# Optimization experiments

Measured on AMD Instinct MI355X. Metric: run time of the kernel, lower is better.

The kernel has to match this reference:

```python
import jax, jax.numpy as jnp
import numpy as np

NH = 16   # n_heads
HD = 64   # head_size
EMB = 1024  # n_embd = NH * HD
B, T = 4, 2048


def setup_inputs() -> dict:
    key = jax.random.key(0)
    k1, k2, k3 = jax.random.split(key, 3)
    x = jax.random.normal(k1, (B, T, EMB), dtype=jnp.float32)
    # torch Linear(in, out, bias=False): weight [out,in]; we store transposed [in,out]
    W_attn = jax.random.normal(k2, (EMB, 3 * NH * HD), dtype=jnp.float32) * (EMB ** -0.5)
    W_proj = jax.random.normal(k3, (NH * HD, EMB), dtype=jnp.float32) * ((NH * HD) ** -0.5)
    b_proj = jnp.zeros((EMB,), dtype=jnp.float32)
    return {"x": x, "W_attn": W_attn, "W_proj": W_proj, "b_proj": b_proj}


def reference(x, W_attn, W_proj, b_proj):
    Bq, Tq, C = x.shape
    qkv = x @ W_attn                      # [B,T,3*Nh*H]
    qs, ks, vs = jnp.split(qkv, 3, axis=2)
    def to_heads(t):                      # [B,T,Nh*H] -> [B,Nh,T,H]
        return t.reshape(Bq, Tq, NH, HD).transpose(0, 2, 1, 3)
    q, k, v = to_heads(qs), to_heads(ks), to_heads(vs)
    scores = jnp.einsum('bnth,bnsh->bnts', q, k) * (HD ** -0.5)  # [B,Nh,T,T]
    causal = jnp.tril(jnp.ones((Tq, Tq), dtype=bool))
    scores = jnp.where(causal, scores, -jnp.inf)
    attn = jax.nn.softmax(scores, axis=-1)
    # dropout is identity in eval mode
    y = jnp.einsum('bnts,bnsh->bnth', attn, v)                   # [B,Nh,T,H]
    y = y.transpose(0, 2, 1, 3).reshape(Bq, Tq, NH * HD)
    return y @ W_proj + b_proj
```

## Files before the change

kernel.cpp:

```cpp
#include <hip/hip_runtime.h>
#include <hip/hip_bf16.h>

#define NH 16
#define HD 64
#define EMB 1024
#define BB 4
#define TT 2048
#define MTOT (BB*TT)
#define N1 (3*NH*HD)
#define KD EMB

#define BM 128
#define BN 128
#define BK 32

typedef __bf16 bf16x8 __attribute__((ext_vector_type(8)));
typedef __bf16 bf16x4 __attribute__((ext_vector_type(4)));
typedef float  f32x4  __attribute__((ext_vector_type(4)));
typedef __hip_bfloat16 hbf;

__device__ __forceinline__ void async_copy16(const hbf* g, hbf* l) {
    __builtin_amdgcn_global_load_lds(
        (const __attribute__((address_space(1))) void*)g,
        (__attribute__((address_space(3))) void*)l, 16, 0, 0);
}

__device__ __forceinline__ bf16x4 pack4(float x0, float x1, float x2, float x3) {
    union { bf16x4 v; hbf a[4]; } u;
    u.a[0] = __float2bfloat16(x0);
    u.a[1] = __float2bfloat16(x1);
    u.a[2] = __float2bfloat16(x2);
    u.a[3] = __float2bfloat16(x3);
    return u.v;
}


__global__ void f32_to_bf16(const float* __restrict__ in, hbf* __restrict__ out, int n) {
    int i = blockIdx.x * blockDim.x + threadIdx.x;
    if (i < n) out[i] = __float2bfloat16(in[i]);
}

__global__ void f32_to_bf16_T(const float* __restrict__ in, hbf* __restrict__ out, int R, int C) {
    int i = blockIdx.x * blockDim.x + threadIdx.x;
    if (i < R * C) {
        int r = i / C, c = i % C;
        out[(size_t)c * R + r] = __float2bfloat16(in[i]);
    }
}


#define GEMM_STAGE(Sdst, Gsrc, ld)                                            \
    {                                                                         \
        _Pragma("unroll")                                                     \
        for (int q = 0; q < 2; ++q) {                                         \
            int e = q * 2048 + tid * 8;                                       \
            int row = e >> 5, col = e & 31;                                   \
            async_copy16(Gsrc + (size_t)row * (ld) + col,                     \
                         Sdst + q * 2048 + (tid & ~63) * 8);                  \
        }                                                                     \
    }

__global__ __launch_bounds__(256) void gemm_qkv(
    const hbf* __restrict__ A, const hbf* __restrict__ Bt,
    hbf* __restrict__ qh, hbf* __restrict__ kh, hbf* __restrict__ vt)
{
    __shared__ __align__(16) hbf As[BM * BK];
    __shared__ __align__(16) hbf Bs[BN * BK];
    int tid = threadIdx.x;
    int wv = tid >> 6, lane = tid & 63;
    int g = lane >> 4, c = lane & 15;
    int wr = wv >> 1, wc = wv & 1;
    int bn = blockIdx.x % (N1 / BN);
    int bm = blockIdx.x / (N1 / BN);
    int m0 = bm * BM, n0 = bn * BN;

    f32x4 acc[4][4];
    #pragma unroll
    for (int i = 0; i < 4; ++i)
        #pragma unroll
        for (int j = 0; j < 4; ++j) acc[i][j] = (f32x4){0.f, 0.f, 0.f, 0.f};

    for (int k0 = 0; k0 < KD; k0 += BK) {
        const hbf* Ag = A  + (size_t)m0 * KD + k0;
        const hbf* Bg = Bt + (size_t)n0 * KD + k0;
        GEMM_STAGE(As, Ag, KD);
        GEMM_STAGE(Bs, Bg, KD);
        __syncthreads();
        bf16x8 af[4], bf[4];
        #pragma unroll
        for (int mi = 0; mi < 4; ++mi)
            af[mi] = *(const bf16x8*)(As + (wr * 64 + mi * 16 + c) * BK + g * 8);
        #pragma unroll
        for (int ni = 0; ni < 4; ++ni)
            bf[ni] = *(const bf16x8*)(Bs + (wc * 64 + ni * 16 + c) * BK + g * 8);
        #pragma unroll
        for (int mi = 0; mi < 4; ++mi)
            #pragma unroll
            for (int ni = 0; ni < 4; ++ni)
                acc[mi][ni] = __builtin_amdgcn_mfma_f32_16x16x32_bf16(af[mi], bf[ni], acc[mi][ni], 0, 0, 0);
        __syncthreads();
    }

    int colbase = n0 + wc * 64;
    int which = colbase / (NH * HD);
    int h = (colbase % (NH * HD)) / HD;
    int b = m0 / TT;
    float scale = (which == 0) ? 0.125f : 1.0f;
    if (which < 2) {
        hbf* dst = (which == 0) ? qh : kh;
        dst += ((size_t)b * NH + h) * TT * HD;
        #pragma unroll
        for (int mi = 0; mi < 4; ++mi)
            #pragma unroll
            for (int ni = 0; ni < 4; ++ni) {
                int d = ni * 16 + c;
                #pragma unroll
                for (int r = 0; r < 4; ++r) {
                    int t = (m0 + wr * 64 + mi * 16 + g * 4 + r) % TT;
                    dst[(size_t)t * HD + d] = __float2bfloat16(acc[mi][ni][r] * scale);
                }
            }
    } else {
        hbf* dst = vt + ((size_t)b * NH + h) * TT * HD;
        #pragma unroll
        for (int mi = 0; mi < 4; ++mi)
            #pragma unroll
            for (int ni = 0; ni < 4; ++ni) {
                int d = ni * 16 + c;
                #pragma unroll
                for (int r = 0; r < 4; ++r) {
                    int t = (m0 + wr * 64 + mi * 16 + g * 4 + r) % TT;
                    dst[(size_t)d * TT + t] = __float2bfloat16(acc[mi][ni][r]);
                }
            }
    }
}


__global__ __launch_bounds__(256, 2) void attn(
    const hbf* __restrict__ qh, const hbf* __restrict__ kh, const hbf* __restrict__ vt,
    hbf* __restrict__ y)
{
    __shared__ __align__(16) hbf Ks[64 * 64];
    __shared__ __align__(16) hbf Vs[64 * 64];
    __shared__ __align__(16) hbf Ps[4][2][16 * 64];

    int tid = threadIdx.x;
    int wv = tid >> 6, lane = tid & 63;
    int g = lane >> 4, c = lane & 15;
    int c7 = c & 7;

    int bh = blockIdx.x >> 3;
    int pi = blockIdx.x & 7;
    int b = bh >> 4, h = bh & 15;

    const hbf* Q = qh + (size_t)bh * TT * HD;
    const hbf* K = kh + (size_t)bh * TT * HD;
    const hbf* V = vt + (size_t)bh * TT * HD;

    #pragma unroll
    for (int pass = 0; pass < 2; ++pass) {
        int sst = pass ? (15 - pi) : pi;
        int qb = sst * 128;
        int qA = qb + wv * 32;
        int qB = qA + 16;
        int kendA = qA + 16, kendB = qA + 32;
        int kmax = qb + 128;

        bf16x8 aqA0 = *(const bf16x8*)(Q + (size_t)(qA + c) * HD + g * 8);
        bf16x8 aqA1 = *(const bf16x8*)(Q + (size_t)(qA + c) * HD + 32 + g * 8);
        bf16x8 aqB0 = *(const bf16x8*)(Q + (size_t)(qB + c) * HD + g * 8);
        bf16x8 aqB1 = *(const bf16x8*)(Q + (size_t)(qB + c) * HD + 32 + g * 8);

        float m_s[2] = {-1e30f, -1e30f}, l_s[2] = {0.f, 0.f};
        f32x4 o[2][4];
        #pragma unroll
        for (int qi = 0; qi < 2; ++qi)
            #pragma unroll
            for (int d = 0; d < 4; ++d) o[qi][d] = (f32x4){0.f, 0.f, 0.f, 0.f};

        for (int k0 = 0; k0 < kmax; k0 += 64) {
            __syncthreads();
            #pragma unroll
            for (int it = 0; it < 2; ++it) {
                int e = it * 2048 + tid * 8;
                int key = e >> 6, sblk = (e >> 3) & 7;
                int dblk = sblk ^ (key & 7);
                async_copy16(K + (size_t)(k0 + key) * HD + dblk * 8,
                             Ks + it * 2048 + (tid & ~63) * 8);
            }
            #pragma unroll
            for (int it = 0; it < 2; ++it) {
                int e = it * 2048 + tid * 8;
                int dim = e >> 6, sblk = (e >> 3) & 7;
                int kb = sblk ^ (dim & 7);
                async_copy16(V + (size_t)dim * TT + k0 + kb * 8,
                             Vs + it * 2048 + (tid & ~63) * 8);
            }
            __syncthreads();

            if (k0 < kendB) {
                f32x4 s[2][4];
                #pragma unroll
                for (int t = 0; t < 4; ++t) {
                    int kt = k0 + 16 * t;
                    if (kt < kendB) {
                        int rb = (16 * t + c) * 64;
                        bf16x8 kf0 = *(const bf16x8*)(Ks + rb + ((g ^ c7) << 3));
                        bf16x8 kf1 = *(const bf16x8*)(Ks + rb + (((4 + g) ^ c7) << 3));
                        if (kt < kendA) {
                            f32x4 a0 = (f32x4){0.f, 0.f, 0.f, 0.f};
                            a0 = __builtin_amdgcn_mfma_f32_16x16x32_bf16(kf0, aqA0, a0, 0, 0, 0);
                            a0 = __builtin_amdgcn_mfma_f32_16x16x32_bf16(kf1, aqA1, a0, 0, 0, 0);
                            if (kt == qA) {
                                #pragma unroll
                                for (int r = 0; r < 4; ++r)
                                    a0[r] = (g * 4 + r <= c) ? a0[r] : -1e30f;
                            }
                            s[0][t] = a0;
                        } else
                            s[0][t] = (f32x4){-1e30f, -1e30f, -1e30f, -1e30f};
                        f32x4 a1 = (f32x4){0.f, 0.f, 0.f, 0.f};
                        a1 = __builtin_amdgcn_mfma_f32_16x16x32_bf16(kf0, aqB0, a1, 0, 0, 0);
                        a1 = __builtin_amdgcn_mfma_f32_16x16x32_bf16(kf1, aqB1, a1, 0, 0, 0);
                        if (kt == qB) {
                            #pragma unroll
                            for (int r = 0; r < 4; ++r)
                                a1[r] = (g * 4 + r <= c) ? a1[r] : -1e30f;
                        }
                        s[1][t] = a1;
                    } else {
                        s[0][t] = (f32x4){-1e30f, -1e30f, -1e30f, -1e30f};
                        s[1][t] = (f32x4){-1e30f, -1e30f, -1e30f, -1e30f};
                    }
                }
                #pragma unroll
                for (int qi = 0; qi < 2; ++qi) {
                    int kend = qi ? kendB : kendA;
                    if (k0 < kend) {
                        f32x4 vmax = s[qi][0];
                        #pragma unroll
                        for (int t = 1; t < 4; ++t)
                            #pragma unroll
                            for (int r = 0; r < 4; ++r)
                                vmax[r] = fmaxf(vmax[r], s[qi][t][r]);
                        float mx = fmaxf(fmaxf(vmax[0], vmax[1]), fmaxf(vmax[2], vmax[3]));
                        mx = fmaxf(mx, __shfl_xor(mx, 16));
                        mx = fmaxf(mx, __shfl_xor(mx, 32));
                        float mn = fmaxf(m_s[qi], mx);
                        float al = __expf(m_s[qi] - mn);
                        m_s[qi] = mn;
                        f32x4 vsum = (f32x4){0.f, 0.f, 0.f, 0.f};
                        hbf* Pq = &Ps[wv][qi][0];
                        #pragma unroll
                        for (int t = 0; t < 4; ++t) {
                            f32x4 e;
                            #pragma unroll
                            for (int r = 0; r < 4; ++r) e[r] = __expf(s[qi][t][r] - mn);
                            vsum += e;
                            *(bf16x4*)(Pq + c * 64 + (((2 * t + (g >> 1)) ^ c7) << 3) + ((g & 1) << 2)) =
                                pack4(e[0], e[1], e[2], e[3]);
                        }
                        float sum = vsum[0] + vsum[1] + vsum[2] + vsum[3];
                        sum += __shfl_xor(sum, 16);
                        sum += __shfl_xor(sum, 32);
                        l_s[qi] = l_s[qi] * al + sum;
                        #pragma unroll
                        for (int d = 0; d < 4; ++d)
                            #pragma unroll
                            for (int r = 0; r < 4; ++r) o[qi][d][r] *= al;
                    }
                }
                #pragma unroll
                for (int sc = 0; sc < 2; ++sc) {
                    int kc = k0 + 32 * sc;
                    if (kc < kendB) {
                        bool lA = kc < kendA;
                        bf16x8 pfB = *(const bf16x8*)(&Ps[wv][1][0] + c * 64 + (((4 * sc + g) ^ c7) << 3));
                        bf16x8 pfA;
                        if (lA)
                            pfA = *(const bf16x8*)(&Ps[wv][0][0] + c * 64 + (((4 * sc + g) ^ c7) << 3));
                        #pragma unroll
                        for (int d = 0; d < 4; ++d) {
                            int dim = d * 16 + c;
                            bf16x8 vf = *(const bf16x8*)(Vs + dim * 64 + (((4 * sc + g) ^ c7) << 3));
                            if (lA)
                                o[0][d] = __builtin_amdgcn_mfma_f32_16x16x32_bf16(vf, pfA, o[0][d], 0, 0, 0);
                            o[1][d] = __builtin_amdgcn_mfma_f32_16x16x32_bf16(vf, pfB, o[1][d], 0, 0, 0);
                        }
                    }
                }
            }
        }

        #pragma unroll
        for (int qi = 0; qi < 2; ++qi) {
            int q0 = qA + qi * 16;
            float inv = 1.0f / l_s[qi];
            #pragma unroll
            for (int d = 0; d < 4; ++d) {
                *(bf16x4*)(y + (size_t)(b * TT + q0 + c) * EMB + h * HD + d * 16 + g * 4) =
                    pack4(o[qi][d][0] * inv, o[qi][d][1] * inv,
                          o[qi][d][2] * inv, o[qi][d][3] * inv);
            }
        }
    }
}


__global__ __launch_bounds__(256) void gemm_out(
    const hbf* __restrict__ A, const hbf* __restrict__ Bt,
    const float* __restrict__ bias, float* __restrict__ out)
{
    __shared__ __align__(16) hbf As[BM * BK];
    __shared__ __align__(16) hbf Bs[BN * BK];
    int tid = threadIdx.x;
    int wv = tid >> 6, lane = tid & 63;
    int g = lane >> 4, c = lane & 15;
    int wr = wv >> 1, wc = wv & 1;
    int bn = blockIdx.x % (EMB / BN);
    int bm = blockIdx.x / (EMB / BN);
    int m0 = bm * BM, n0 = bn * BN;

    f32x4 acc[4][4];
    #pragma unroll
    for (int i = 0; i < 4; ++i)
        #pragma unroll
        for (int j = 0; j < 4; ++j) acc[i][j] = (f32x4){0.f, 0.f, 0.f, 0.f};

    for (int k0 = 0; k0 < EMB; k0 += BK) {
        const hbf* Ag = A  + (size_t)m0 * EMB + k0;
        const hbf* Bg = Bt + (size_t)n0 * EMB + k0;
        GEMM_STAGE(As, Ag, EMB);
        GEMM_STAGE(Bs, Bg, EMB);
        __syncthreads();
        bf16x8 af[4], bf[4];
        #pragma unroll
        for (int mi = 0; mi < 4; ++mi)
            af[mi] = *(const bf16x8*)(As + (wr * 64 + mi * 16 + c) * BK + g * 8);
        #pragma unroll
        for (int ni = 0; ni < 4; ++ni)
            bf[ni] = *(const bf16x8*)(Bs + (wc * 64 + ni * 16 + c) * BK + g * 8);
        #pragma unroll
        for (int mi = 0; mi < 4; ++mi)
            #pragma unroll
            for (int ni = 0; ni < 4; ++ni)
                acc[mi][ni] = __builtin_amdgcn_mfma_f32_16x16x32_bf16(af[mi], bf[ni], acc[mi][ni], 0, 0, 0);
        __syncthreads();
    }

    #pragma unroll
    for (int mi = 0; mi < 4; ++mi)
        #pragma unroll
        for (int ni = 0; ni < 4; ++ni) {
            int col = n0 + wc * 64 + ni * 16 + c;
            float bv = bias[col];
            #pragma unroll
            for (int r = 0; r < 4; ++r) {
                int row = m0 + wr * 64 + mi * 16 + g * 4 + r;
                out[(size_t)row * EMB + col] = acc[mi][ni][r] + bv;
            }
        }
}


extern "C" void kernel_launch(void* const* d_in, const int* in_sizes, int n_in,
                              void* d_out, int out_size, void* d_ws, size_t ws_size,
                              hipStream_t stream)
{
    const float* x      = (const float*)d_in[0];
    const float* W_attn = (const float*)d_in[1];
    const float* W_proj = (const float*)d_in[2];
    const float* b_proj = (const float*)d_in[3];
    float* out = (float*)d_out;

    char* ws = (char*)d_ws;
    hbf* xb    = (hbf*)ws; ws += (size_t)MTOT * KD * 2;
    hbf* wab_t = (hbf*)ws; ws += (size_t)N1 * KD * 2;
    hbf* wpb_t = (hbf*)ws; ws += (size_t)EMB * EMB * 2;
    hbf* qh    = (hbf*)ws; ws += (size_t)MTOT * EMB * 2;
    hbf* kh    = (hbf*)ws; ws += (size_t)MTOT * EMB * 2;
    hbf* vt    = (hbf*)ws; ws += (size_t)MTOT * EMB * 2;
    hbf* yb    = (hbf*)ws; ws += (size_t)MTOT * EMB * 2;

    f32_to_bf16<<<(MTOT * KD + 255) / 256, 256, 0, stream>>>(x, xb, MTOT * KD);
    f32_to_bf16_T<<<(KD * N1 + 255) / 256, 256, 0, stream>>>(W_attn, wab_t, KD, N1);
    f32_to_bf16_T<<<(KD * EMB + 255) / 256, 256, 0, stream>>>(W_proj, wpb_t, KD, EMB);

    gemm_qkv<<<(MTOT / BM) * (N1 / BN), 256, 0, stream>>>(xb, wab_t, qh, kh, vt);
    attn<<<BB * NH * 8, 256, 0, stream>>>(qh, kh, vt, yb);
    gemm_out<<<(MTOT / BM) * (EMB / BN), 256, 0, stream>>>(yb, wpb_t, b_proj, out);
}
```

Measured before the change: 290.0 us.

## Retile attention to 64-query blocks with 128-key tiles and vectorize conversions

```diff
diff --git a/kernel.cpp b/kernel.cpp
--- a/kernel.cpp
+++ b/kernel.cpp
@@ -14,6 +14,8 @@
 #define BN 128
 #define BK 32
 
+#define QSCALE 0.18033688011112042f
+
 typedef __bf16 bf16x8 __attribute__((ext_vector_type(8)));
 typedef __bf16 bf16x4 __attribute__((ext_vector_type(4)));
 typedef float  f32x4  __attribute__((ext_vector_type(4)));
@@ -26,26 +28,35 @@
 }
 
 __device__ __forceinline__ bf16x4 pack4(float x0, float x1, float x2, float x3) {
-    union { bf16x4 v; hbf a[4]; } u;
-    u.a[0] = __float2bfloat16(x0);
-    u.a[1] = __float2bfloat16(x1);
-    u.a[2] = __float2bfloat16(x2);
-    u.a[3] = __float2bfloat16(x3);
+    union { bf16x4 v; __hip_bfloat162 h[2]; } u;
+    u.h[0] = __float22bfloat162_rn(float2{x0, x1});
+    u.h[1] = __float22bfloat162_rn(float2{x2, x3});
     return u.v;
 }
 
 
-__global__ void f32_to_bf16(const float* __restrict__ in, hbf* __restrict__ out, int n) {
+__global__ __launch_bounds__(256) void f32_to_bf16_v4(const float* __restrict__ in,
+                                                      hbf* __restrict__ out, int n4) {
     int i = blockIdx.x * blockDim.x + threadIdx.x;
-    if (i < n) out[i] = __float2bfloat16(in[i]);
-}
-
-__global__ void f32_to_bf16_T(const float* __restrict__ in, hbf* __restrict__ out, int R, int C) {
-    int i = blockIdx.x * blockDim.x + threadIdx.x;
-    if (i < R * C) {
-        int r = i / C, c = i % C;
-        out[(size_t)c * R + r] = __float2bfloat16(in[i]);
-    }
+    if (i < n4) {
+        float4 v = ((const float4*)in)[i];
+        *(bf16x4*)(out + 4 * (size_t)i) = pack4(v.x, v.y, v.z, v.w);
+    }
+}
+
+__global__ __launch_bounds__(256) void f32_to_bf16_T(const float* __restrict__ in,
+                                                     hbf* __restrict__ out, int R, int C) {
+    __shared__ float T[64][65];
+    int bc = blockIdx.x % (C / 64), br = blockIdx.x / (C / 64);
+    int r0 = br * 64, c0 = bc * 64;
+    int tr = threadIdx.x >> 6, tc = threadIdx.x & 63;
+    #pragma unroll
+    for (int i = 0; i < 16; ++i)
+        T[4 * i + tr][tc] = in[(size_t)(r0 + 4 * i + tr) * C + c0 + tc];
+    __syncthreads();
+    #pragma unroll
+    for (int i = 0; i < 16; ++i)
+        out[(size_t)(c0 + 4 * i + tr) * R + r0 + tc] = __float2bfloat16(T[tc][4 * i + tr]);
 }
 
 
@@ -105,7 +116,7 @@
     int which = colbase / (NH * HD);
     int h = (colbase % (NH * HD)) / HD;
     int b = m0 / TT;
-    float scale = (which == 0) ? 0.125f : 1.0f;
+    float scale = (which == 0) ? QSCALE : 1.0f;
     if (which < 2) {
         hbf* dst = (which == 0) ? qh : kh;
         dst += ((size_t)b * NH + h) * TT * HD;
@@ -137,35 +148,49 @@
 }
 
 
-__global__ __launch_bounds__(256, 2) void attn(
+__global__ __launch_bounds__(128, 2) void attn(
     const hbf* __restrict__ qh, const hbf* __restrict__ kh, const hbf* __restrict__ vt,
     hbf* __restrict__ y)
 {
-    __shared__ __align__(16) hbf Ks[64 * 64];
-    __shared__ __align__(16) hbf Vs[64 * 64];
-    __shared__ __align__(16) hbf Ps[4][2][16 * 64];
+    __shared__ __align__(16) hbf Ks[128 * 64];
+    __shared__ __align__(16) hbf Vs[2 * 64 * 64];
+    __shared__ __align__(16) hbf Ps[2][2][16 * 64];
 
     int tid = threadIdx.x;
     int wv = tid >> 6, lane = tid & 63;
     int g = lane >> 4, c = lane & 15;
     int c7 = c & 7;
 
-    int bh = blockIdx.x >> 3;
-    int pi = blockIdx.x & 7;
+    int bh = blockIdx.x >> 4;
+    int pi = blockIdx.x & 15;
     int b = bh >> 4, h = bh & 15;
 
     const hbf* Q = qh + (size_t)bh * TT * HD;
     const hbf* K = kh + (size_t)bh * TT * HD;
     const hbf* V = vt + (size_t)bh * TT * HD;
+    hbf* PqA = &Ps[wv][0][0];
+    hbf* PqB = &Ps[wv][1][0];
+
+    int koff[8], voff[8];
+    #pragma unroll
+    for (int it = 0; it < 8; ++it) {
+        int e = it * 1024 + tid * 8;
+        int key = e >> 6, sblk = (e >> 3) & 7;
+        koff[it] = key * HD + ((sblk ^ (key & 7)) << 3);
+        int ch = e >> 12, rem = e & 4095;
+        int dim = rem >> 6, kb8 = (rem >> 3) & 7;
+        voff[it] = dim * TT + ch * 64 + ((kb8 ^ (dim & 7)) << 3);
+    }
+    int ldsb = (tid & ~63) * 8;
 
     #pragma unroll
     for (int pass = 0; pass < 2; ++pass) {
-        int sst = pass ? (15 - pi) : pi;
-        int qb = sst * 128;
+        int sst = pass ? (31 - pi) : pi;
+        int qb = sst * 64;
         int qA = qb + wv * 32;
         int qB = qA + 16;
         int kendA = qA + 16, kendB = qA + 32;
-        int kmax = qb + 128;
+        int kmax = qb + 64;
 
         bf16x8 aqA0 = *(const bf16x8*)(Q + (size_t)(qA + c) * HD + g * 8);
         bf16x8 aqA1 = *(const bf16x8*)(Q + (size_t)(qA + c) * HD + 32 + g * 8);
@@ -179,114 +204,111 @@
             #pragma unroll
             for (int d = 0; d < 4; ++d) o[qi][d] = (f32x4){0.f, 0.f, 0.f, 0.f};
 
-        for (int k0 = 0; k0 < kmax; k0 += 64) {
+        for (int k0 = 0; k0 < kmax; k0 += 128) {
             __syncthreads();
             #pragma unroll
-            for (int it = 0; it < 2; ++it) {
-                int e = it * 2048 + tid * 8;
-                int key = e >> 6, sblk = (e >> 3) & 7;
-                int dblk = sblk ^ (key & 7);
-                async_copy16(K + (size_t)(k0 + key) * HD + dblk * 8,
-                             Ks + it * 2048 + (tid & ~63) * 8);
-            }
-            #pragma unroll
-            for (int it = 0; it < 2; ++it) {
-                int e = it * 2048 + tid * 8;
-                int dim = e >> 6, sblk = (e >> 3) & 7;
-                int kb = sblk ^ (dim & 7);
-                async_copy16(V + (size_t)dim * TT + k0 + kb * 8,
-                             Vs + it * 2048 + (tid & ~63) * 8);
-            }
+            for (int it = 0; it < 8; ++it)
+                async_copy16(K + (size_t)k0 * HD + koff[it], Ks + it * 1024 + ldsb);
+            #pragma unroll
+            for (int it = 0; it < 8; ++it)
+                async_copy16(V + k0 + voff[it], Vs + it * 1024 + ldsb);
             __syncthreads();
 
-            if (k0 < kendB) {
-                f32x4 s[2][4];
-                #pragma unroll
-                for (int t = 0; t < 4; ++t) {
-                    int kt = k0 + 16 * t;
-                    if (kt < kendB) {
-                        int rb = (16 * t + c) * 64;
-                        bf16x8 kf0 = *(const bf16x8*)(Ks + rb + ((g ^ c7) << 3));
-                        bf16x8 kf1 = *(const bf16x8*)(Ks + rb + (((4 + g) ^ c7) << 3));
-                        if (kt < kendA) {
-                            f32x4 a0 = (f32x4){0.f, 0.f, 0.f, 0.f};
-                            a0 = __builtin_amdgcn_mfma_f32_16x16x32_bf16(kf0, aqA0, a0, 0, 0, 0);
-                            a0 = __builtin_amdgcn_mfma_f32_16x16x32_bf16(kf1, aqA1, a0, 0, 0, 0);
-                            if (kt == qA) {
+            #pragma unroll
+            for (int ch = 0; ch < 2; ++ch) {
+                int c64 = k0 + ch * 64;
+                if (c64 < kendB) {
+                    f32x4 s[2][4];
+                    #pragma unroll
+                    for (int t = 0; t < 4; ++t) {
+                        int kt = c64 + 16 * t;
+                        if (kt < kendB) {
+                            int rb = (ch * 64 + 16 * t + c) * 64;
+                            bf16x8 kf0 = *(const bf16x8*)(Ks + rb + ((g ^ c7) << 3));
+                            bf16x8 kf1 = *(const bf16x8*)(Ks + rb + (((4 + g) ^ c7) << 3));
+                            if (kt < kendA) {
+                                f32x4 a = (f32x4){0.f, 0.f, 0.f, 0.f};
+                                a = __builtin_amdgcn_mfma_f32_16x16x32_bf16(kf0, aqA0, a, 0, 0, 0);
+                                a = __builtin_amdgcn_mfma_f32_16x16x32_bf16(kf1, aqA1, a, 0, 0, 0);
+                                if (kt == qA) {
+                                    #pragma unroll
+                                    for (int r = 0; r < 4; ++r)
+                                        a[r] = (g * 4 + r <= c) ? a[r] : -1e30f;
+                                }
+                                s[0][t] = a;
+                            } else
+                                s[0][t] = (f32x4){-1e30f, -1e30f, -1e30f, -1e30f};
+                            f32x4 a1 = (f32x4){0.f, 0.f, 0.f, 0.f};
+                            a1 = __builtin_amdgcn_mfma_f32_16x16x32_bf16(kf0, aqB0, a1, 0, 0, 0);
+                            a1 = __builtin_amdgcn_mfma_f32_16x16x32_bf16(kf1, aqB1, a1, 0, 0, 0);
+                            if (kt == qB) {
                                 #pragma unroll
                                 for (int r = 0; r < 4; ++r)
-                                    a0[r] = (g * 4 + r <= c) ? a0[r] : -1e30f;
+                                    a1[r] = (g * 4 + r <= c) ? a1[r] : -1e30f;
                             }
-                            s[0][t] = a0;
-                        } else
+                            s[1][t] = a1;
+                        } else {
                             s[0][t] = (f32x4){-1e30f, -1e30f, -1e30f, -1e30f};
-                        f32x4 a1 = (f32x4){0.f, 0.f, 0.f, 0.f};
-                        a1 = __builtin_amdgcn_mfma_f32_16x16x32_bf16(kf0, aqB0, a1, 0, 0, 0);
-                        a1 = __builtin_amdgcn_mfma_f32_16x16x32_bf16(kf1, aqB1, a1, 0, 0, 0);
-                        if (kt == qB) {
+                            s[1][t] = (f32x4){-1e30f, -1e30f, -1e30f, -1e30f};
+                        }
+                    }
+                    #pragma unroll
+                    for (int qi = 0; qi < 2; ++qi) {
+                        int kend = qi ? kendB : kendA;
+                        if (c64 < kend) {
+                            f32x4 vmax = s[qi][0];
                             #pragma unroll
-                            for (int r = 0; r < 4; ++r)
-                                a1[r] = (g * 4 + r <= c) ? a1[r] : -1e30f;
+                            for (int t = 1; t < 4; ++t)
+                                #pragma unroll
+                                for (int r = 0; r < 4; ++r)
+                                    vmax[r] = fmaxf(vmax[r], s[qi][t][r]);
+                            float mx = fmaxf(fmaxf(vmax[0], vmax[1]), fmaxf(vmax[2], vmax[3]));
+                            mx = fmaxf(mx, __shfl_xor(mx, 16));
+                            mx = fmaxf(mx, __shfl_xor(mx, 32));
+                            float mn = fmaxf(m_s[qi], mx);
+                            float al = exp2f(m_s[qi] - mn);
+                            m_s[qi] = mn;
+                            f32x4 vsum = (f32x4){0.f, 0.f, 0.f, 0.f};
+                            hbf* Pq = qi ? PqB : PqA;
+                            #pragma unroll
+                            for (int t = 0; t < 4; ++t) {
+                                f32x4 e;
+                                #pragma unroll
+                                for (int r = 0; r < 4; ++r) e[r] = exp2f(s[qi][t][r] - mn);
+                                vsum += e;
+                                *(bf16x4*)(Pq + c * 64 + (((2 * t + (g >> 1)) ^ c7) << 3) + ((g & 1) << 2)) =
+                                    pack4(e[0], e[1], e[2], e[3]);
+                            }
+                            float sum = vsum[0] + vsum[1] + vsum[2] + vsum[3];
+                            sum += __shfl_xor(sum, 16);
+                            sum += __shfl_xor(sum, 32);
+                            l_s[qi] = l_s[qi] * al + sum;
+                            if (__any(al != 1.0f)) {
+                                #pragma unroll
+                                for (int d = 0; d < 4; ++d)
+                                    #pragma unroll
+                                    for (int r = 0; r < 4; ++r) o[qi][d][r] *= al;
+                            }
                         }
-                        s[1][t] = a1;
-                    } else {
-                        s[0][t] = (f32x4){-1e30f, -1e30f, -1e30f, -1e30f};
-                        s[1][t] = (f32x4){-1e30f, -1e30f, -1e30f, -1e30f};
                     }
-                }
-                #pragma unroll
-                for (int qi = 0; qi < 2; ++qi) {
-                    int kend = qi ? kendB : kendA;
-                    if (k0 < kend) {
-                        f32x4 vmax = s[qi][0];
-                        #pragma unroll
-                        for (int t = 1; t < 4; ++t)
+                    #pragma unroll
+                    for (int sc = 0; sc < 2; ++sc) {
+                        int kc = c64 + 32 * sc;
+                        if (kc < kendB) {
+                            bool lA = kc < kendA;
+                            bf16x8 pfB = *(const bf16x8*)(PqB + c * 64 + (((4 * sc + g) ^ c7) << 3));
+                            bf16x8 pfA;
+                            if (lA)
+                                pfA = *(const bf16x8*)(PqA + c * 64 + (((4 * sc + g) ^ c7) << 3));
                             #pragma unroll
-                            for (int r = 0; r < 4; ++r)
-                                vmax[r] = fmaxf(vmax[r], s[qi][t][r]);
-                        float mx = fmaxf(fmaxf(vmax[0], vmax[1]), fmaxf(vmax[2], vmax[3]));
-                        mx = fmaxf(mx, __shfl_xor(mx, 16));
-                        mx = fmaxf(mx, __shfl_xor(mx, 32));
-                        float mn = fmaxf(m_s[qi], mx);
-                        float al = __expf(m_s[qi] - mn);
-                        m_s[qi] = mn;
-                        f32x4 vsum = (f32x4){0.f, 0.f, 0.f, 0.f};
-                        hbf* Pq = &Ps[wv][qi][0];
-                        #pragma unroll
-                        for (int t = 0; t < 4; ++t) {
-                            f32x4 e;
-                            #pragma unroll
-                            for (int r = 0; r < 4; ++r) e[r] = __expf(s[qi][t][r] - mn);
-                            vsum += e;
-                            *(bf16x4*)(Pq + c * 64 + (((2 * t + (g >> 1)) ^ c7) << 3) + ((g & 1) << 2)) =
-                                pack4(e[0], e[1], e[2], e[3]);
-                        }
-                        float sum = vsum[0] + vsum[1] + vsum[2] + vsum[3];
-                        sum += __shfl_xor(sum, 16);
-                        sum += __shfl_xor(sum, 32);
-                        l_s[qi] = l_s[qi] * al + sum;
-                        #pragma unroll
-                        for (int d = 0; d < 4; ++d)
-                            #pragma unroll
-                            for (int r = 0; r < 4; ++r) o[qi][d][r] *= al;
-                    }
-                }
-                #pragma unroll
-                for (int sc = 0; sc < 2; ++sc) {
-                    int kc = k0 + 32 * sc;
-                    if (kc < kendB) {
-                        bool lA = kc < kendA;
-                        bf16x8 pfB = *(const bf16x8*)(&Ps[wv][1][0] + c * 64 + (((4 * sc + g) ^ c7) << 3));
-                        bf16x8 pfA;
-                        if (lA)
-                            pfA = *(const bf16x8*)(&Ps[wv][0][0] + c * 64 + (((4 * sc + g) ^ c7) << 3));
-                        #pragma unroll
-                        for (int d = 0; d < 4; ++d) {
-                            int dim = d * 16 + c;
-                            bf16x8 vf = *(const bf16x8*)(Vs + dim * 64 + (((4 * sc + g) ^ c7) << 3));
-                            if (lA)
-                                o[0][d] = __builtin_amdgcn_mfma_f32_16x16x32_bf16(vf, pfA, o[0][d], 0, 0, 0);
-                            o[1][d] = __builtin_amdgcn_mfma_f32_16x16x32_bf16(vf, pfB, o[1][d], 0, 0, 0);
+                            for (int d = 0; d < 4; ++d) {
+                                int dim = d * 16 + c;
+                                bf16x8 vf = *(const bf16x8*)(Vs + ch * 4096 + dim * 64 +
+                                                             (((4 * sc + g) ^ c7) << 3));
+                                if (lA)
+                                    o[0][d] = __builtin_amdgcn_mfma_f32_16x16x32_bf16(vf, pfA, o[0][d], 0, 0, 0);
+                                o[1][d] = __builtin_amdgcn_mfma_f32_16x16x32_bf16(vf, pfB, o[1][d], 0, 0, 0);
+                            }
                         }
                     }
                 }
@@ -383,11 +405,11 @@
     hbf* vt    = (hbf*)ws; ws += (size_t)MTOT * EMB * 2;
     hbf* yb    = (hbf*)ws; ws += (size_t)MTOT * EMB * 2;
 
-    f32_to_bf16<<<(MTOT * KD + 255) / 256, 256, 0, stream>>>(x, xb, MTOT * KD);
-    f32_to_bf16_T<<<(KD * N1 + 255) / 256, 256, 0, stream>>>(W_attn, wab_t, KD, N1);
-    f32_to_bf16_T<<<(KD * EMB + 255) / 256, 256, 0, stream>>>(W_proj, wpb_t, KD, EMB);
+    f32_to_bf16_v4<<<(MTOT * KD / 4 + 255) / 256, 256, 0, stream>>>(x, xb, MTOT * KD / 4);
+    f32_to_bf16_T<<<(KD / 64) * (N1 / 64), 256, 0, stream>>>(W_attn, wab_t, KD, N1);
+    f32_to_bf16_T<<<(KD / 64) * (EMB / 64), 256, 0, stream>>>(W_proj, wpb_t, KD, EMB);
 
     gemm_qkv<<<(MTOT / BM) * (N1 / BN), 256, 0, stream>>>(xb, wab_t, qh, kh, vt);
-    attn<<<BB * NH * 8, 256, 0, stream>>>(qh, kh, vt, yb);
+    attn<<<BB * NH * 16, 128, 0, stream>>>(qh, kh, vt, yb);
     gemm_out<<<(MTOT / BM) * (EMB / BN), 256, 0, stream>>>(yb, wpb_t, b_proj, out);
 }
```

Measured after the change: 291.9 us. Within noise of the previous version (+0.7%).
